# Kernel optimization log

Hardware: AMD Instinct MI355X
Metric: run time of the kernel (lower is better)

Reference implementation:

```python
import jax, jax.numpy as jnp
import numpy as np
import math

V, H, NH, L, S, B = 100000, 2048, 64, 2, 512, 2
HD = H // NH  # 32
MAX_LEN = 5000
EPS_NORM = 1e-5
EPS_ATTN = 1e-6


def build_pe():
    # PositionalEncoding buffer: pe[max_len, 1, d_model]
    position = jnp.arange(MAX_LEN, dtype=jnp.float32)[:, None]
    div_term = jnp.exp(jnp.arange(0, H, 2, dtype=jnp.float32) * (-math.log(10000.0) / H))
    ang = position * div_term  # [max_len, H/2]
    pe = jnp.zeros((MAX_LEN, 1, H), dtype=jnp.float32)
    pe = pe.at[:, 0, 0::2].set(jnp.sin(ang))
    pe = pe.at[:, 0, 1::2].set(jnp.cos(ang))
    return pe


def fast_inv_sqrt(x):
    # Quake fast inverse sqrt; the bit-trick seed is detached in the original
    x2 = x * 0.5
    i = jax.lax.bitcast_convert_type(jax.lax.stop_gradient(x.astype(jnp.float32)), jnp.int32)
    i = jnp.int32(1597463007) - (i >> 1)
    y = jax.lax.bitcast_convert_type(i, jnp.float32)
    return y * (1.5 - x2 * y * y)  # grad flows only through x2, as in torch


def sr_norm(h, w, b):
    mean = h.mean(-1, keepdims=True)
    var = ((h - mean) ** 2).mean(-1, keepdims=True)  # biased variance
    inv = fast_inv_sqrt(var + EPS_NORM)
    return w * ((h - mean) * inv) + b


def attn_layer(x, wq, bq, wk, bk, wv, bv, wo, bo, nw, nb):
    # x: [B, S, H]; weights stored [in, out]
    def heads(t):
        return t.reshape(B, S, NH, HD).transpose(0, 2, 1, 3)  # [B, NH, S, HD]
    q = heads(x @ wq + bq)
    k = heads(x @ wk + bk)
    v = heads(x @ wv + bv)
    scores = jnp.einsum('bhqd,bhkd->bhqk', q, k) / math.sqrt(HD)
    a = jax.nn.softmax(scores, axis=-1)
    # dropout is identity in eval; then double softmax (exp/sum) + sigmoid gate
    e = jnp.exp(a)
    a2 = e / (e.sum(-1, keepdims=True) + EPS_ATTN)
    cw = a2 * jax.nn.sigmoid(a2)
    o = jnp.einsum('bhqk,bhkd->bhqd', cw, v)
    o = o.transpose(0, 2, 1, 3).reshape(B, S, H)
    o = o @ wo + bo
    return sr_norm(o + x, nw, nb)


def setup_inputs():
    key = jax.random.key(0)
    ks = jax.random.split(key, 12)
    def rn(k, shape):
        return jax.random.normal(k, shape, dtype=jnp.float32) * 0.02
    return {
        'src': jax.random.randint(ks[0], (B, S), 0, V),
        'emb': jax.random.uniform(ks[1], (V, H), minval=-0.1, maxval=0.1, dtype=jnp.float32),
        'Wq': rn(ks[2], (L, H, H)), 'bq': jnp.zeros((L, H), jnp.float32),
        'Wk': rn(ks[3], (L, H, H)), 'bk': jnp.zeros((L, H), jnp.float32),
        'Wv': rn(ks[4], (L, H, H)), 'bv': jnp.zeros((L, H), jnp.float32),
        'Wo': rn(ks[5], (L, H, H)), 'bo': jnp.zeros((L, H), jnp.float32),
        'nw': jnp.ones((L, H), jnp.float32), 'nb': jnp.zeros((L, H), jnp.float32),
        'Wout': jax.random.uniform(ks[6], (H, V), minval=-0.1, maxval=0.1, dtype=jnp.float32),
        'bout': jnp.zeros((V,), jnp.float32),
    }


def reference(src, emb, Wq, bq, Wk, bk, Wv, bv, Wo, bo, nw, nb, Wout, bout):
    x = emb[src] * math.sqrt(H)  # [B, S, H]
    pe = build_pe()
    # Faithful to pe[:x.size(0)] where x is [B, S, H]: indexes by BATCH dim
    x = x + pe[:x.shape[0]]  # [B, 1, H] broadcast over seq
    for l in range(L):
        x = attn_layer(x, Wq[l], bq[l], Wk[l], bk[l], Wv[l], bv[l],
                       Wo[l], bo[l], nw[l], nb[l])
    return x @ Wout + bout  # [B, S, V]
```

## Files before the change

### kernel.cpp

```cpp
#include <hip/hip_runtime.h>


#define DEVINL __device__ __forceinline__

typedef float f32x4 __attribute__((ext_vector_type(4)));
typedef __bf16 bf16x8 __attribute__((ext_vector_type(8)));
typedef __bf16 bf16x2v __attribute__((ext_vector_type(2)));

DEVINL unsigned int pk2(float a, float b) {
  bf16x2v v;
  v[0] = (__bf16)a;
  v[1] = (__bf16)b;
  return __builtin_bit_cast(unsigned int, v);
}

DEVINL unsigned short bf1(float a) {
  __bf16 v = (__bf16)a;
  return __builtin_bit_cast(unsigned short, v);
}

DEVINL void gload_lds16(const void* g, void* l) {
  __builtin_amdgcn_global_load_lds(
      (const __attribute__((address_space(1))) unsigned int*)g,
      (__attribute__((address_space(3))) unsigned int*)l, 16, 0, 0);
}

__global__ __launch_bounds__(256) void embed_kernel(
    const int* __restrict__ src, const float* __restrict__ emb,
    float* __restrict__ x, unsigned short* __restrict__ xbf) {
  const int row = blockIdx.x;
  const int b = row >> 9;
  const int tok = src[row];
  const float sqrtH = 45.25483399593904f;
  const float c = -9.210340371976184f / 2048.f;
  for (int h = threadIdx.x; h < 2048; h += 256) {
    int i = h >> 1;
    float dv = expf((float)(2 * i) * c);
    float ang = (float)b * dv;
    float pe = (h & 1) ? cosf(ang) : sinf(ang);
    float val = emb[(size_t)tok * 2048 + h] * sqrtH + pe;
    x[(size_t)row * 2048 + h] = val;
    xbf[(size_t)row * 2048 + h] = bf1(val);
  }
}

__global__ __launch_bounds__(256) void wtrans_kernel(
    const float* __restrict__ W, unsigned short* __restrict__ WT, const int N) {
  __shared__ float t[64][65];
  const int tid = threadIdx.x;
  const int n0 = blockIdx.x * 64, k0 = blockIdx.y * 64;
#pragma unroll
  for (int i = 0; i < 16; ++i) {
    int kl = i * 4 + (tid >> 6);
    int n = n0 + (tid & 63);
    t[kl][tid & 63] = (n < N) ? W[(size_t)(k0 + kl) * N + n] : 0.f;
  }
  __syncthreads();
#pragma unroll
  for (int j = 0; j < 8; ++j) {
    int nl = j * 8 + (tid >> 5);
    int kp = (tid & 31) * 2;
    unsigned int u = pk2(t[kp][nl], t[kp + 1][nl]);
    *(unsigned int*)&WT[(size_t)(n0 + nl) * 2048 + k0 + kp] = u;
  }
}

template <int BM, int NN>
DEVINL void gemm_bf_body(const unsigned short* __restrict__ A,
                         const unsigned short* __restrict__ BT,
                         const float* __restrict__ bias, float* __restrict__ C,
                         const int m0, const int n0) {
  constexpr int K = 2048;
  constexpr int WM = BM / 32;
  __shared__ __align__(16) unsigned short A_lds[2][BM * 32];
  __shared__ __align__(16) unsigned short B_lds[2][128 * 32];

  const int tid = threadIdx.x;
  const int w = tid >> 6, lane = tid & 63;
  const int wm = w >> 1, wn = w & 1;

  const int aRow = lane >> 2;
  const int aChunk = (lane & 3) ^ ((lane >> 3) & 3);

  int aOff[WM], bOff[4];
#pragma unroll
  for (int mi = 0; mi < WM; ++mi) {
    int m = wm * (BM / 2) + mi * 16 + (lane & 15);
    aOff[mi] = m * 32 + ((lane >> 4) ^ ((m >> 1) & 3)) * 8;
  }
#pragma unroll
  for (int ni = 0; ni < 4; ++ni) {
    int n = wn * 64 + ni * 16 + (lane & 15);
    bOff[ni] = n * 32 + ((lane >> 4) ^ ((n >> 1) & 3)) * 8;
  }

  f32x4 acc[WM][4] = {};

  auto stage = [&](int k0, int bf) {
#pragma unroll
    for (int i = 0; i < BM / 64; ++i) {
      int r0 = (w * (BM / 64) + i) * 16;
      gload_lds16(A + (size_t)(m0 + r0 + aRow) * K + k0 + aChunk * 8, &A_lds[bf][r0 * 32]);
    }
#pragma unroll
    for (int i = 0; i < 2; ++i) {
      int r0 = (w * 2 + i) * 16;
      gload_lds16(BT + (size_t)(n0 + r0 + aRow) * K + k0 + aChunk * 8, &B_lds[bf][r0 * 32]);
    }
  };
  auto compute = [&](int bf) {
    bf16x8 af[WM], bfr[4];
#pragma unroll
    for (int mi = 0; mi < WM; ++mi) af[mi] = *(const bf16x8*)&A_lds[bf][aOff[mi]];
#pragma unroll
    for (int ni = 0; ni < 4; ++ni) bfr[ni] = *(const bf16x8*)&B_lds[bf][bOff[ni]];
#pragma unroll
    for (int mi = 0; mi < WM; ++mi)
#pragma unroll
      for (int ni = 0; ni < 4; ++ni)
        acc[mi][ni] = __builtin_amdgcn_mfma_f32_16x16x32_bf16(af[mi], bfr[ni], acc[mi][ni], 0, 0, 0);
  };

  stage(0, 0);
  __syncthreads();
  int buf = 0;
  for (int t = 0; t < K / 32 - 1; ++t) {
    stage((t + 1) * 32, buf ^ 1);
    compute(buf);
    __syncthreads();
    buf ^= 1;
  }
  compute(buf);

  const int r0w = (lane >> 4) * 4;
  const int lrow = lane & 15;
#pragma unroll
  for (int mi = 0; mi < WM; ++mi)
#pragma unroll
    for (int ni = 0; ni < 4; ++ni) {
      int ccol = n0 + wn * 64 + ni * 16 + lrow;
      if ((NN % 128 == 0) || ccol < NN) {
        float bv = bias[ccol];
#pragma unroll
        for (int r = 0; r < 4; ++r) {
          int crow = m0 + wm * (BM / 2) + mi * 16 + r0w + r;
          C[(size_t)crow * NN + ccol] = acc[mi][ni][r] + bv;
        }
      }
    }
}

template <int BM, int NN>
__global__ __launch_bounds__(256) void gemm_bf_kernel(
    const unsigned short* __restrict__ A, const unsigned short* __restrict__ BT,
    const float* __restrict__ bias, float* __restrict__ C) {
  gemm_bf_body<BM, NN>(A, BT, bias, C, blockIdx.x * BM, blockIdx.y * 128);
}

__global__ __launch_bounds__(256) void gemm_qkv_bf_kernel(
    const unsigned short* __restrict__ A, const unsigned short* __restrict__ WT,
    const float* __restrict__ bq, const float* __restrict__ bk, const float* __restrict__ bv,
    float* __restrict__ q, float* __restrict__ k, float* __restrict__ v) {
  const int z = blockIdx.z;
  const unsigned short* BT = WT + (size_t)z * 2048 * 2048;
  const float* bias = (z == 0) ? bq : (z == 1) ? bk : bv;
  float* C = (z == 0) ? q : (z == 1) ? k : v;
  gemm_bf_body<64, 2048>(A, BT, bias, C, blockIdx.x * 64, blockIdx.y * 128);
}

__global__ __launch_bounds__(256) void gemm_final_bf_kernel(
    const unsigned short* __restrict__ A, const unsigned short* __restrict__ BT,
    const float* __restrict__ bias, float* __restrict__ C) {
  const int bid = blockIdx.x;
  const int f = (bid & 7) * (gridDim.x >> 3) + (bid >> 3);
  gemm_bf_body<128, 100000>(A, BT, bias, C, (f & 7) * 128, (f >> 3) * 128);
}

template <int BM>
DEVINL void gemm_body(const unsigned short* __restrict__ A, const float* __restrict__ B,
                      const float* __restrict__ bias, float* __restrict__ C,
                      const int N, const int m0, const int n0) {
  constexpr int K = 2048;
  constexpr int WM = BM / 32;
  constexpr int AI = BM / 64;
  __shared__ __align__(16) unsigned short A_lds[2][BM * 32];
  __shared__ __align__(16) unsigned short B_lds[2][128 * 32];

  const int tid = threadIdx.x;
  const int w = tid >> 6, lane = tid & 63;
  const int wm = w >> 1, wn = w & 1;

  const int n_local = tid & 127;
  const int kq = tid >> 7;
  const int col = n0 + n_local;
  const bool colok = col < N;
  const int bswz = (n_local >> 1) & 3;

  const int aRow = lane >> 2;
  const int aChunk = (lane & 3) ^ ((lane >> 3) & 3);

  int aOff[WM], bOff[4];
#pragma unroll
  for (int mi = 0; mi < WM; ++mi) {
    int m = wm * (BM / 2) + mi * 16 + (lane & 15);
    aOff[mi] = m * 32 + ((lane >> 4) ^ ((m >> 1) & 3)) * 8;
  }
#pragma unroll
  for (int ni = 0; ni < 4; ++ni) {
    int n = wn * 64 + ni * 16 + (lane & 15);
    bOff[ni] = n * 32 + ((lane >> 4) ^ ((n >> 1) & 3)) * 8;
  }

  f32x4 acc[WM][4] = {};
  float fB[16];

  auto stageA = [&](int k0, int bf) {
#pragma unroll
    for (int i = 0; i < AI; ++i) {
      int r0 = (w * AI + i) * 16;
      gload_lds16(A + (size_t)(m0 + r0 + aRow) * K + k0 + aChunk * 8, &A_lds[bf][r0 * 32]);
    }
  };
  auto loadB = [&](int k0) {
#pragma unroll
    for (int g = 0; g < 4; ++g) {
      int kl = (g * 2 + kq) * 4;
#pragma unroll
      for (int i = 0; i < 4; ++i)
        fB[g * 4 + i] = colok ? B[(size_t)(k0 + kl + i) * N + col] : 0.f;
    }
  };
  auto writeB = [&](int bf) {
#pragma unroll
    for (int g = 0; g < 4; ++g) {
      int kl = (g * 2 + kq) * 4;
      uint2 p = make_uint2(pk2(fB[g * 4 + 0], fB[g * 4 + 1]),
                           pk2(fB[g * 4 + 2], fB[g * 4 + 3]));
      int chunk = (kl >> 3) ^ bswz;
      *(uint2*)&B_lds[bf][n_local * 32 + chunk * 8 + (kl & 7)] = p;
    }
  };
  auto compute = [&](int bf) {
    bf16x8 af[WM], bfr[4];
#pragma unroll
    for (int mi = 0; mi < WM; ++mi) af[mi] = *(const bf16x8*)&A_lds[bf][aOff[mi]];
#pragma unroll
    for (int ni = 0; ni < 4; ++ni) bfr[ni] = *(const bf16x8*)&B_lds[bf][bOff[ni]];
#pragma unroll
    for (int mi = 0; mi < WM; ++mi)
#pragma unroll
      for (int ni = 0; ni < 4; ++ni)
        acc[mi][ni] = __builtin_amdgcn_mfma_f32_16x16x32_bf16(af[mi], bfr[ni], acc[mi][ni], 0, 0, 0);
  };

  stageA(0, 0);
  loadB(0);
  writeB(0);
  __syncthreads();
  int buf = 0;
  for (int t = 0; t < K / 32 - 1; ++t) {
    stageA((t + 1) * 32, buf ^ 1);
    loadB((t + 1) * 32);
    compute(buf);
    writeB(buf ^ 1);
    __syncthreads();
    buf ^= 1;
  }
  compute(buf);

  const int r0w = (lane >> 4) * 4;
  const int lrow = lane & 15;
#pragma unroll
  for (int mi = 0; mi < WM; ++mi)
#pragma unroll
    for (int ni = 0; ni < 4; ++ni) {
      int ccol = n0 + wn * 64 + ni * 16 + lrow;
      if (ccol < N) {
        float bv = bias[ccol];
#pragma unroll
        for (int r = 0; r < 4; ++r) {
          int crow = m0 + wm * (BM / 2) + mi * 16 + r0w + r;
          C[(size_t)crow * N + ccol] = acc[mi][ni][r] + bv;
        }
      }
    }
}

__global__ __launch_bounds__(256) void gemm_qkv_kernel(
    const unsigned short* __restrict__ A,
    const float* __restrict__ Wq, const float* __restrict__ Wk, const float* __restrict__ Wv,
    const float* __restrict__ bq, const float* __restrict__ bk, const float* __restrict__ bv,
    float* __restrict__ q, float* __restrict__ k, float* __restrict__ v) {
  const int z = blockIdx.z;
  const float* B = (z == 0) ? Wq : (z == 1) ? Wk : Wv;
  const float* bias = (z == 0) ? bq : (z == 1) ? bk : bv;
  float* C = (z == 0) ? q : (z == 1) ? k : v;
  gemm_body<64>(A, B, bias, C, 2048, blockIdx.x * 64, blockIdx.y * 128);
}

template <int BM>
__global__ __launch_bounds__(256) void gemm_kernel(
    const unsigned short* __restrict__ A, const float* __restrict__ B,
    const float* __restrict__ bias, float* __restrict__ C, const int N) {
  gemm_body<BM>(A, B, bias, C, N, blockIdx.x * BM, blockIdx.y * 128);
}

__global__ __launch_bounds__(256) void gemm_final_kernel(
    const unsigned short* __restrict__ A, const float* __restrict__ B,
    const float* __restrict__ bias, float* __restrict__ C, const int N) {
  const int bid = blockIdx.x;
  const int f = (bid & 7) * (gridDim.x >> 3) + (bid >> 3);
  gemm_body<128>(A, B, bias, C, N, (f & 7) * 128, (f >> 3) * 128);
}

__global__ __launch_bounds__(256) void attn_kernel(
    const float* __restrict__ q, const float* __restrict__ k,
    const float* __restrict__ v, unsigned short* __restrict__ o) {
  __shared__ __align__(16) float K_lds[512 * 32];
  const int tid = threadIdx.x;
  const int blk = blockIdx.x;
  const int bh = blk >> 1, chunk = blk & 1;
  const int b = bh >> 6, h = bh & 63;
  const size_t headoff = (size_t)b * 512 * 2048 + (size_t)h * 32;

  const float* kb = k + headoff;
#pragma unroll
  for (int i = 0; i < 16; ++i) {
    int flat = i * 256 + tid;
    int j = flat >> 3, d4 = flat & 7;
    *(float4*)&K_lds[j * 32 + d4 * 4] = *(const float4*)(kb + (size_t)j * 2048 + d4 * 4);
  }
  __syncthreads();

  const int row = chunk * 256 + tid;
  const float* qr = q + headoff + (size_t)row * 2048;
  float4 Q[8];
#pragma unroll
  for (int d = 0; d < 8; ++d) Q[d] = *(const float4*)(qr + d * 4);

  const float scale = 0.17677669529663689f;
  auto dot = [&](int j) -> float {
    const float4* kr = (const float4*)&K_lds[j * 32];
    float p0 = 0.f, p1 = 0.f, p2 = 0.f, p3 = 0.f;
#pragma unroll
    for (int d = 0; d < 8; ++d) {
      float4 kk = kr[d];
      p0 = fmaf(Q[d].x, kk.x, p0);
      p1 = fmaf(Q[d].y, kk.y, p1);
      p2 = fmaf(Q[d].z, kk.z, p2);
      p3 = fmaf(Q[d].w, kk.w, p3);
    }
    return ((p0 + p1) + (p2 + p3)) * scale;
  };

  float m = -1e30f, denom = 0.f;
  for (int j = 0; j < 512; ++j) {
    float s = dot(j);
    float nm = fmaxf(m, s);
    denom = denom * __expf(m - nm) + __expf(s - nm);
    m = nm;
  }
  const float invd = 1.f / denom;

  float sum_e = 0.f;
  for (int j = 0; j < 512; ++j) {
    float a = __expf(dot(j) - m) * invd;
    sum_e += __expf(a);
  }
  const float inv_se = 1.f / (sum_e + 1e-6f);

  float4 accv[8];
#pragma unroll
  for (int d = 0; d < 8; ++d) accv[d] = make_float4(0.f, 0.f, 0.f, 0.f);
  const float* vb = v + headoff;
  float4 vcur[8];
#pragma unroll
  for (int d = 0; d < 8; ++d) vcur[d] = ((const float4*)vb)[d];
  for (int j = 0; j < 512; ++j) {
    float4 vnxt[8];
    if (j < 511) {
      const float4* vr = (const float4*)(vb + (size_t)(j + 1) * 2048);
#pragma unroll
      for (int d = 0; d < 8; ++d) vnxt[d] = vr[d];
    } else {
#pragma unroll
      for (int d = 0; d < 8; ++d) vnxt[d] = vcur[d];
    }
    float a = __expf(dot(j) - m) * invd;
    float e = __expf(a);
    float a2 = e * inv_se;
    float cw = a2 / (1.f + __expf(-a2));
#pragma unroll
    for (int d = 0; d < 8; ++d) {
      accv[d].x = fmaf(cw, vcur[d].x, accv[d].x);
      accv[d].y = fmaf(cw, vcur[d].y, accv[d].y);
      accv[d].z = fmaf(cw, vcur[d].z, accv[d].z);
      accv[d].w = fmaf(cw, vcur[d].w, accv[d].w);
    }
#pragma unroll
    for (int d = 0; d < 8; ++d) vcur[d] = vnxt[d];
  }
  unsigned short* orow = o + headoff + (size_t)row * 2048;
#pragma unroll
  for (int d = 0; d < 8; ++d) {
    uint2 p = make_uint2(pk2(accv[d].x, accv[d].y), pk2(accv[d].z, accv[d].w));
    *(uint2*)&orow[d * 4] = p;
  }
}

__global__ __launch_bounds__(256) void norm_kernel(
    const float* __restrict__ o, const float* __restrict__ xin,
    const float* __restrict__ w, const float* __restrict__ bb,
    float* __restrict__ xout, unsigned short* __restrict__ xbf) {
  __shared__ float red[4];
  const int row = blockIdx.x, tid = threadIdx.x;
  const float* op = o + (size_t)row * 2048;
  const float* xp = xin + (size_t)row * 2048;
  float4 hv[2];
#pragma unroll
  for (int i = 0; i < 2; ++i) {
    float4 a = *(const float4*)(op + tid * 4 + i * 1024);
    float4 c = *(const float4*)(xp + tid * 4 + i * 1024);
    hv[i] = make_float4(a.x + c.x, a.y + c.y, a.z + c.z, a.w + c.w);
  }
  float s = 0.f;
#pragma unroll
  for (int i = 0; i < 2; ++i) s += hv[i].x + hv[i].y + hv[i].z + hv[i].w;
  for (int off = 32; off; off >>= 1) s += __shfl_down(s, off);
  if ((tid & 63) == 0) red[tid >> 6] = s;
  __syncthreads();
  const float mean = (red[0] + red[1] + red[2] + red[3]) * (1.f / 2048.f);
  __syncthreads();

  float vs = 0.f;
#pragma unroll
  for (int i = 0; i < 2; ++i) {
    float dx = hv[i].x - mean, dy = hv[i].y - mean, dz = hv[i].z - mean, dw = hv[i].w - mean;
    vs += dx * dx + dy * dy + dz * dz + dw * dw;
  }
  for (int off = 32; off; off >>= 1) vs += __shfl_down(vs, off);
  if ((tid & 63) == 0) red[tid >> 6] = vs;
  __syncthreads();
  const float var = (red[0] + red[1] + red[2] + red[3]) * (1.f / 2048.f);

  const float xv = var + 1e-5f;
  int ii = __float_as_int(xv);
  ii = 1597463007 - (ii >> 1);
  float y = __int_as_float(ii);
  y = y * (1.5f - 0.5f * xv * y * y);

#pragma unroll
  for (int i = 0; i < 2; ++i) {
    int c0 = tid * 4 + i * 1024;
    float4 wv = *(const float4*)(w + c0);
    float4 bv = *(const float4*)(bb + c0);
    float r0 = wv.x * ((hv[i].x - mean) * y) + bv.x;
    float r1 = wv.y * ((hv[i].y - mean) * y) + bv.y;
    float r2 = wv.z * ((hv[i].z - mean) * y) + bv.z;
    float r3 = wv.w * ((hv[i].w - mean) * y) + bv.w;
    *(float4*)(xout + (size_t)row * 2048 + c0) = make_float4(r0, r1, r2, r3);
    *(uint2*)&xbf[(size_t)row * 2048 + c0] = make_uint2(pk2(r0, r1), pk2(r2, r3));
  }
}

extern "C" void kernel_launch(void* const* d_in, const int* in_sizes, int n_in,
                              void* d_out, int out_size, void* d_ws, size_t ws_size,
                              hipStream_t stream) {
  const int*   src  = (const int*)d_in[0];
  const float* emb  = (const float*)d_in[1];
  const float* Wq   = (const float*)d_in[2];
  const float* bq   = (const float*)d_in[3];
  const float* Wk   = (const float*)d_in[4];
  const float* bk   = (const float*)d_in[5];
  const float* Wv   = (const float*)d_in[6];
  const float* bv   = (const float*)d_in[7];
  const float* Wo   = (const float*)d_in[8];
  const float* bo   = (const float*)d_in[9];
  const float* nw   = (const float*)d_in[10];
  const float* nb   = (const float*)d_in[11];
  const float* Wout = (const float*)d_in[12];
  const float* bout = (const float*)d_in[13];
  float* out = (float*)d_out;

  char* ws = (char*)d_ws;
  float* x  = (float*)(ws);
  float* qb = (float*)(ws + (8ll << 20));
  float* kb = (float*)(ws + (16ll << 20));
  float* vb = (float*)(ws + (24ll << 20));
  float* ob = (float*)(ws + (32ll << 20));
  unsigned short* xbf = (unsigned short*)(ws + (40ll << 20));
  unsigned short* abf = (unsigned short*)(ws + (44ll << 20));

  const unsigned long long NEED = (112ull << 20) + 100096ull * 2048ull * 2ull;
  const bool big = (unsigned long long)ws_size >= NEED;
  unsigned short* WTp = (unsigned short*)(ws + (48ll << 20));
  unsigned short* WTo = (unsigned short*)(ws + (112ll << 20));

  embed_kernel<<<1024, 256, 0, stream>>>(src, emb, x, xbf);

  if (big) {
    for (int l = 0; l < 2; ++l) {
      const size_t wo_ = (size_t)l * 2048 * 2048;
      const float* Wm[4] = {Wq + wo_, Wk + wo_, Wv + wo_, Wo + wo_};
      for (int mt = 0; mt < 4; ++mt)
        wtrans_kernel<<<dim3(32, 32), 256, 0, stream>>>(
            Wm[mt], WTp + (size_t)(l * 4 + mt) * 2048 * 2048, 2048);
    }
    wtrans_kernel<<<dim3(1564, 32), 256, 0, stream>>>(Wout, WTo, 100000);

    for (int l = 0; l < 2; ++l) {
      const size_t bo_ = (size_t)l * 2048;
      const unsigned short* WTl = WTp + (size_t)(l * 4) * 2048 * 2048;
      gemm_qkv_bf_kernel<<<dim3(16, 16, 3), 256, 0, stream>>>(
          xbf, WTl, bq + bo_, bk + bo_, bv + bo_, qb, kb, vb);
      attn_kernel<<<256, 256, 0, stream>>>(qb, kb, vb, abf);
      gemm_bf_kernel<64, 2048><<<dim3(16, 16), 256, 0, stream>>>(
          abf, WTl + (size_t)3 * 2048 * 2048, bo + bo_, ob);
      norm_kernel<<<1024, 256, 0, stream>>>(ob, x, nw + bo_, nb + bo_, x, xbf);
    }
    gemm_final_bf_kernel<<<8 * 782, 256, 0, stream>>>(xbf, WTo, bout, out);
  } else {
    for (int l = 0; l < 2; ++l) {
      const size_t wo_ = (size_t)l * 2048 * 2048;
      const size_t bo_ = (size_t)l * 2048;
      gemm_qkv_kernel<<<dim3(16, 16, 3), 256, 0, stream>>>(
          xbf, Wq + wo_, Wk + wo_, Wv + wo_, bq + bo_, bk + bo_, bv + bo_, qb, kb, vb);
      attn_kernel<<<256, 256, 0, stream>>>(qb, kb, vb, abf);
      gemm_kernel<64><<<dim3(16, 16), 256, 0, stream>>>(abf, Wo + wo_, bo + bo_, ob, 2048);
      norm_kernel<<<1024, 256, 0, stream>>>(ob, x, nw + bo_, nb + bo_, x, xbf);
    }
    gemm_final_kernel<<<8 * 782, 256, 0, stream>>>(xbf, Wout, bout, out, 100000);
  }
}
```

Before: 1.962 ms.

## Split attention keys across thread pairs and vectorize weight transpose loads

The attention kernel now gives each query row to two threads, each covering half of the 512 keys. The partial max/denominator, exp-sum and output accumulators are merged with lane shuffles, and the grid doubles to 512 blocks. This aims to double parallelism across the GPU's compute units and halve the serial loop length per thread, at the cost of more K loads per block and shuffle merges. Separately, the weight transpose kernel now reads float4 and writes 8-byte packed bf16 stores to cut memory instructions, with a scalar fallback at the edges.

Result: faster. 1.839 ms (-6.3%).

```diff
diff --git a/kernel.cpp b/kernel.cpp
--- a/kernel.cpp
+++ b/kernel.cpp
@@ -49,19 +49,33 @@
   __shared__ float t[64][65];
   const int tid = threadIdx.x;
   const int n0 = blockIdx.x * 64, k0 = blockIdx.y * 64;
-#pragma unroll
-  for (int i = 0; i < 16; ++i) {
-    int kl = i * 4 + (tid >> 6);
-    int n = n0 + (tid & 63);
-    t[kl][tid & 63] = (n < N) ? W[(size_t)(k0 + kl) * N + n] : 0.f;
-  }
-  __syncthreads();
-#pragma unroll
-  for (int j = 0; j < 8; ++j) {
-    int nl = j * 8 + (tid >> 5);
-    int kp = (tid & 31) * 2;
-    unsigned int u = pk2(t[kp][nl], t[kp + 1][nl]);
-    *(unsigned int*)&WT[(size_t)(n0 + nl) * 2048 + k0 + kp] = u;
+  const int c4 = (tid & 15) * 4;
+#pragma unroll
+  for (int it = 0; it < 4; ++it) {
+    int kl = it * 16 + (tid >> 4);
+    int n = n0 + c4;
+    float4 wv;
+    if (n + 3 < N) {
+      wv = *(const float4*)(W + (size_t)(k0 + kl) * N + n);
+    } else {
+      wv.x = (n + 0 < N) ? W[(size_t)(k0 + kl) * N + n + 0] : 0.f;
+      wv.y = (n + 1 < N) ? W[(size_t)(k0 + kl) * N + n + 1] : 0.f;
+      wv.z = (n + 2 < N) ? W[(size_t)(k0 + kl) * N + n + 2] : 0.f;
+      wv.w = (n + 3 < N) ? W[(size_t)(k0 + kl) * N + n + 3] : 0.f;
+    }
+    t[kl][c4 + 0] = wv.x;
+    t[kl][c4 + 1] = wv.y;
+    t[kl][c4 + 2] = wv.z;
+    t[kl][c4 + 3] = wv.w;
+  }
+  __syncthreads();
+  const int kp = (tid & 15) * 4;
+#pragma unroll
+  for (int j = 0; j < 4; ++j) {
+    int nl = j * 16 + (tid >> 4);
+    uint2 u = make_uint2(pk2(t[kp + 0][nl], t[kp + 1][nl]),
+                         pk2(t[kp + 2][nl], t[kp + 3][nl]));
+    *(uint2*)&WT[(size_t)(n0 + nl) * 2048 + k0 + kp] = u;
   }
 }
 
@@ -319,7 +333,7 @@
   __shared__ __align__(16) float K_lds[512 * 32];
   const int tid = threadIdx.x;
   const int blk = blockIdx.x;
-  const int bh = blk >> 1, chunk = blk & 1;
+  const int bh = blk >> 2, chunk = blk & 3;
   const int b = bh >> 6, h = bh & 63;
   const size_t headoff = (size_t)b * 512 * 2048 + (size_t)h * 32;
 
@@ -332,7 +346,9 @@
   }
   __syncthreads();
 
-  const int row = chunk * 256 + tid;
+  const int row = chunk * 128 + (tid >> 1);
+  const int half = tid & 1;
+  const int j0 = half * 256, j1 = j0 + 256;
   const float* qr = q + headoff + (size_t)row * 2048;
   float4 Q[8];
 #pragma unroll
@@ -354,19 +370,27 @@
   };
 
   float m = -1e30f, denom = 0.f;
-  for (int j = 0; j < 512; ++j) {
+  for (int j = j0; j < j1; ++j) {
     float s = dot(j);
     float nm = fmaxf(m, s);
     denom = denom * __expf(m - nm) + __expf(s - nm);
     m = nm;
   }
+  {
+    float m2 = __shfl_xor(m, 1);
+    float d2 = __shfl_xor(denom, 1);
+    float mm = fmaxf(m, m2);
+    denom = denom * __expf(m - mm) + d2 * __expf(m2 - mm);
+    m = mm;
+  }
   const float invd = 1.f / denom;
 
   float sum_e = 0.f;
-  for (int j = 0; j < 512; ++j) {
+  for (int j = j0; j < j1; ++j) {
     float a = __expf(dot(j) - m) * invd;
     sum_e += __expf(a);
   }
+  sum_e += __shfl_xor(sum_e, 1);
   const float inv_se = 1.f / (sum_e + 1e-6f);
 
   float4 accv[8];
@@ -375,10 +399,10 @@
   const float* vb = v + headoff;
   float4 vcur[8];
 #pragma unroll
-  for (int d = 0; d < 8; ++d) vcur[d] = ((const float4*)vb)[d];
-  for (int j = 0; j < 512; ++j) {
+  for (int d = 0; d < 8; ++d) vcur[d] = *(const float4*)(vb + (size_t)j0 * 2048 + d * 4);
+  for (int j = j0; j < j1; ++j) {
     float4 vnxt[8];
-    if (j < 511) {
+    if (j + 1 < j1) {
       const float4* vr = (const float4*)(vb + (size_t)(j + 1) * 2048);
 #pragma unroll
       for (int d = 0; d < 8; ++d) vnxt[d] = vr[d];
@@ -400,9 +424,17 @@
 #pragma unroll
     for (int d = 0; d < 8; ++d) vcur[d] = vnxt[d];
   }
+#pragma unroll
+  for (int d = 0; d < 8; ++d) {
+    accv[d].x += __shfl_xor(accv[d].x, 1);
+    accv[d].y += __shfl_xor(accv[d].y, 1);
+    accv[d].z += __shfl_xor(accv[d].z, 1);
+    accv[d].w += __shfl_xor(accv[d].w, 1);
+  }
   unsigned short* orow = o + headoff + (size_t)row * 2048;
 #pragma unroll
-  for (int d = 0; d < 8; ++d) {
+  for (int g = 0; g < 4; ++g) {
+    int d = half * 4 + g;
     uint2 p = make_uint2(pk2(accv[d].x, accv[d].y), pk2(accv[d].z, accv[d].w));
     *(uint2*)&orow[d * 4] = p;
   }
@@ -513,7 +545,7 @@
       const unsigned short* WTl = WTp + (size_t)(l * 4) * 2048 * 2048;
       gemm_qkv_bf_kernel<<<dim3(16, 16, 3), 256, 0, stream>>>(
           xbf, WTl, bq + bo_, bk + bo_, bv + bo_, qb, kb, vb);
-      attn_kernel<<<256, 256, 0, stream>>>(qb, kb, vb, abf);
+      attn_kernel<<<512, 256, 0, stream>>>(qb, kb, vb, abf);
       gemm_bf_kernel<64, 2048><<<dim3(16, 16), 256, 0, stream>>>(
           abf, WTl + (size_t)3 * 2048 * 2048, bo + bo_, ob);
       norm_kernel<<<1024, 256, 0, stream>>>(ob, x, nw + bo_, nb + bo_, x, xbf);
@@ -525,7 +557,7 @@
       const size_t bo_ = (size_t)l * 2048;
       gemm_qkv_kernel<<<dim3(16, 16, 3), 256, 0, stream>>>(
           xbf, Wq + wo_, Wk + wo_, Wv + wo_, bq + bo_, bk + bo_, bv + bo_, qb, kb, vb);
-      attn_kernel<<<256, 256, 0, stream>>>(qb, kb, vb, abf);
+      attn_kernel<<<512, 256, 0, stream>>>(qb, kb, vb, abf);
       gemm_kernel<64><<<dim3(16, 16), 256, 0, stream>>>(abf, Wo + wo_, bo + bo_, ob, 2048);
       norm_kernel<<<1024, 256, 0, stream>>>(ob, x, nw + bo_, nb + bo_, x, xbf);
     }
```
